# Kernel tuning notes

Hardware: AMD Instinct MI355X
Metric: run time of the kernel (lower is better)

Reference implementation:

```python
import jax, jax.numpy as jnp
import numpy as np


def setup_inputs() -> dict:
    key = jax.random.key(0)
    k = jax.random.split(key, 5)
    B, Cin, Cout, H, W = 16, 32, 32, 256, 256
    m1, m2 = 16, 16
    scale = (1.0 / (Cin * Cout)) ** 0.5  # RandomUniform limit in original
    x = jax.random.normal(k[0], (B, Cin, H, W), dtype=jnp.float32)
    ws = {
        'w1_real': jax.random.uniform(k[1], (Cin, Cout, m1, m2), jnp.float32, -scale, scale),
        'w1_imag': jax.random.uniform(k[2], (Cin, Cout, m1, m2), jnp.float32, -scale, scale),
        'w2_real': jax.random.uniform(k[3], (Cin, Cout, m1, m2), jnp.float32, -scale, scale),
        'w2_imag': jax.random.uniform(k[4], (Cin, Cout, m1, m2), jnp.float32, -scale, scale),
    }
    return {'x': x, **ws}


def reference(x, w1_real, w1_imag, w2_real, w2_imag):
    B, Cin, H, W = x.shape
    Cout, m1, m2 = w1_real.shape[1], w1_real.shape[2], w1_real.shape[3]
    Wr = W // 2 + 1
    # full rFFT2 over (H, W); x_ft: [B, Cin, H, Wr] complex64
    x_ft = jnp.fft.rfft2(x, axes=(-2, -1))
    w1 = w1_real + 1j * w1_imag  # [Cin, Cout, m1, m2]
    w2 = w2_real + 1j * w2_imag
    top = jnp.einsum('bixy,ioxy->boxy', x_ft[:, :, :m1, :m2], w1)
    bottom = jnp.einsum('bixy,ioxy->boxy', x_ft[:, :, -m1:, :m2], w2)
    out_ft = jnp.zeros((B, Cout, H, Wr), dtype=x_ft.dtype)
    out_ft = out_ft.at[:, :, :m1, :m2].set(top)
    # original pads bottom block to start at row h_ft - m1 and ADDS the two padded tensors
    out_ft = out_ft.at[:, :, H - m1:, :m2].add(bottom)
    return jnp.fft.irfft2(out_ft, s=(H, W), axes=(-2, -1))
```

## Files before the change

kernel.cpp:

```cpp
#include <hip/hip_runtime.h>
#include <math.h>


#define TWO_PI_256 0.0245436926f

typedef short short8 __attribute__((ext_vector_type(8)));
typedef float f32x4  __attribute__((ext_vector_type(4)));

__device__ __forceinline__ ushort f2bf(float v) {
    unsigned u = __float_as_uint(v);
    u += 0x7FFFu + ((u >> 16) & 1u);
    return (ushort)(u >> 16);
}
__device__ __forceinline__ float bf2f(ushort h) {
    return __uint_as_float(((unsigned)h) << 16);
}

__global__ void init_frags(ushort* __restrict__ Fr) {
    const int s = blockIdx.x;
    const int lane = threadIdx.x;
    const int q = lane >> 4, n = lane & 15;
    for (int j = 0; j < 8; ++j) {
        float v = 0.f;
        int hl;
        if (s < 32) {
            int tn = s >> 4; hl = (s >> 3) & 1; int ch = s & 7;
            int w = ch * 32 + q * 8 + j, ky = n;
            float sn, cs; __sincosf((float)((w * ky) & 255) * TWO_PI_256, &sn, &cs);
            v = tn == 0 ? cs : -sn;
        } else if (s < 160) {
            int s2 = s - 32; int mt = s2 >> 5; hl = (s2 >> 4) & 1; int ch = s2 & 15;
            int m = mt * 16 + n, k = ch * 32 + q * 8 + j;
            int kxi = m >> 1, rx = m & 1, h = k >> 1, rt = k & 1;
            int r = kxi + (kxi >= 16 ? 224 : 0);
            float sn, cs; __sincosf((float)((r * h) & 255) * TWO_PI_256, &sn, &cs);
            v = (rx == 0) ? (rt == 0 ? cs : sn) : (rt == 0 ? -sn : cs);
        } else if (s < 288) {
            int s3 = s - 160; int mtG = s3 >> 2; hl = (s3 >> 1) & 1; int ch = s3 & 1;
            int m = mtG * 16 + n, k = ch * 32 + q * 8 + j;
            int h = m >> 1, rg = m & 1, kxi = k >> 1, ry = k & 1;
            int r = kxi + (kxi >= 16 ? 224 : 0);
            float sn, cs; __sincosf((float)((r * h) & 255) * TWO_PI_256, &sn, &cs);
            v = ((rg == 0) ? (ry == 0 ? cs : -sn) : (ry == 0 ? sn : cs)) * (1.0f / 65536.0f);
        } else {
            int s4 = s - 288; int nt = s4 >> 1; hl = s4 & 1;
            int k = q * 8 + j, w = nt * 16 + n;
            int ky = k >> 1, ri = k & 1;
            float sn, cs; __sincosf((float)((w * ky) & 255) * TWO_PI_256, &sn, &cs);
            v = (ky == 0) ? (ri ? 0.f : 1.f) : (ri ? -2.f * sn : 2.f * cs);
        }
        ushort hi = f2bf(v);
        Fr[s * 512 + lane * 8 + j] = hl == 0 ? hi : f2bf(v - bf2f(hi));
    }
}

__global__ __launch_bounds__(256) void f1_gemm(const float* __restrict__ x,
                                               const ushort* __restrict__ Fr,
                                               float* __restrict__ T) {
    __shared__ ushort Ah[128 * 32], Al[128 * 32];
    const int t = threadIdx.x, blk = blockIdx.x;
    const size_t row0 = (size_t)blk * 128;
    const int bi = blk >> 1, h0 = (blk & 1) * 128;
    const int srow = t >> 3, sw4 = t & 7;
    const int lane = t & 63, wid = t >> 6, q = lane >> 4, n = lane & 15;

    f32x4 acc[2][2];
    #pragma unroll
    for (int a = 0; a < 2; ++a)
        #pragma unroll
        for (int b = 0; b < 2; ++b) acc[a][b] = (f32x4){0.f, 0.f, 0.f, 0.f};

    for (int ch = 0; ch < 8; ++ch) {
        __syncthreads();
        #pragma unroll
        for (int m = 0; m < 4; ++m) {
            const int row = srow + 32 * m;
            float4 v = *(const float4*)(x + (row0 + row) * 256 + ch * 32 + sw4 * 4);
            ushort h0_ = f2bf(v.x), h1 = f2bf(v.y), h2 = f2bf(v.z), h3 = f2bf(v.w);
            *(ushort4*)&Ah[row * 32 + sw4 * 4] = make_ushort4(h0_, h1, h2, h3);
            *(ushort4*)&Al[row * 32 + sw4 * 4] = make_ushort4(f2bf(v.x - bf2f(h0_)), f2bf(v.y - bf2f(h1)),
                                                              f2bf(v.z - bf2f(h2)), f2bf(v.w - bf2f(h3)));
        }
        __syncthreads();

        short8 bh0 = *(const short8*)&Fr[(size_t)(0  + ch) * 512 + lane * 8];
        short8 bl0 = *(const short8*)&Fr[(size_t)(8  + ch) * 512 + lane * 8];
        short8 bh1 = *(const short8*)&Fr[(size_t)(16 + ch) * 512 + lane * 8];
        short8 bl1 = *(const short8*)&Fr[(size_t)(24 + ch) * 512 + lane * 8];

        #pragma unroll
        for (int mt = 0; mt < 2; ++mt) {
            const int row = wid * 32 + mt * 16 + n;
            short8 ah = *(const short8*)&Ah[row * 32 + q * 8];
            short8 al = *(const short8*)&Al[row * 32 + q * 8];
            acc[mt][0] = __builtin_amdgcn_mfma_f32_16x16x32_bf16(al, bh0, acc[mt][0], 0, 0, 0);
            acc[mt][0] = __builtin_amdgcn_mfma_f32_16x16x32_bf16(ah, bl0, acc[mt][0], 0, 0, 0);
            acc[mt][0] = __builtin_amdgcn_mfma_f32_16x16x32_bf16(ah, bh0, acc[mt][0], 0, 0, 0);
            acc[mt][1] = __builtin_amdgcn_mfma_f32_16x16x32_bf16(al, bh1, acc[mt][1], 0, 0, 0);
            acc[mt][1] = __builtin_amdgcn_mfma_f32_16x16x32_bf16(ah, bl1, acc[mt][1], 0, 0, 0);
            acc[mt][1] = __builtin_amdgcn_mfma_f32_16x16x32_bf16(ah, bh1, acc[mt][1], 0, 0, 0);
        }
    }
    #pragma unroll
    for (int tn = 0; tn < 2; ++tn)
        #pragma unroll
        for (int mt = 0; mt < 2; ++mt)
            #pragma unroll
            for (int r = 0; r < 4; ++r) {
                int h = h0 + wid * 32 + mt * 16 + q * 4 + r;
                T[(size_t)((h * 2 + tn) * 512 + bi) * 16 + n] = acc[mt][tn][r];
            }
}

__global__ __launch_bounds__(256) void f2_gemm(const float* __restrict__ T,
                                               const ushort* __restrict__ Fr,
                                               float* __restrict__ X) {
    __shared__ ushort Bs[8 * 512];
    const int t = threadIdx.x;
    const int n0 = blockIdx.x * 64;
    const int lane = t & 63, wid = t >> 6, q = lane >> 4, nn = lane & 15;
    const int kk = t >> 3, ne = (t & 7) * 8, qk = kk >> 3, jk = kk & 7;

    f32x4 acc[4];
    #pragma unroll
    for (int m = 0; m < 4; ++m) acc[m] = (f32x4){0.f, 0.f, 0.f, 0.f};

    for (int ch = 0; ch < 16; ++ch) {
        __syncthreads();
        {
            float v[8];
            *(float4*)&v[0] = *(const float4*)&T[(size_t)(ch * 32 + kk) * 8192 + n0 + ne];
            *(float4*)&v[4] = *(const float4*)&T[(size_t)(ch * 32 + kk) * 8192 + n0 + ne + 4];
            #pragma unroll
            for (int e = 0; e < 8; ++e) {
                int nc = ne + e, nt = nc >> 4, lf = qk * 16 + (nc & 15);
                ushort hi = f2bf(v[e]);
                Bs[(nt * 2 + 0) * 512 + lf * 8 + jk] = hi;
                Bs[(nt * 2 + 1) * 512 + lf * 8 + jk] = f2bf(v[e] - bf2f(hi));
            }
        }
        __syncthreads();
        short8 bh = *(const short8*)&Bs[(wid * 2 + 0) * 512 + lane * 8];
        short8 bl = *(const short8*)&Bs[(wid * 2 + 1) * 512 + lane * 8];
        #pragma unroll
        for (int mt = 0; mt < 4; ++mt) {
            short8 ah = *(const short8*)&Fr[(size_t)(32 + mt * 32 + ch) * 512 + lane * 8];
            short8 al = *(const short8*)&Fr[(size_t)(32 + mt * 32 + 16 + ch) * 512 + lane * 8];
            acc[mt] = __builtin_amdgcn_mfma_f32_16x16x32_bf16(al, bh, acc[mt], 0, 0, 0);
            acc[mt] = __builtin_amdgcn_mfma_f32_16x16x32_bf16(ah, bl, acc[mt], 0, 0, 0);
            acc[mt] = __builtin_amdgcn_mfma_f32_16x16x32_bf16(ah, bh, acc[mt], 0, 0, 0);
        }
    }
    const int col = n0 + wid * 16 + nn;
    #pragma unroll
    for (int mt = 0; mt < 4; ++mt)
        #pragma unroll
        for (int r = 0; r < 4; ++r)
            X[(size_t)(mt * 16 + q * 4 + r) * 8192 + col] = acc[mt][r];
}

__global__ __launch_bounds__(256) void mix(const float* __restrict__ X,
                                           const float* __restrict__ w1r_, const float* __restrict__ w1i_,
                                           const float* __restrict__ w2r_, const float* __restrict__ w2i_,
                                           float* __restrict__ Y) {
    int gid = blockIdx.x * 256 + threadIdx.x;
    int ky = gid & 15, kxi = (gid >> 4) & 31, o = (gid >> 9) & 31, b = gid >> 14;
    const float* wr = (kxi < 16) ? w1r_ : w2r_;
    const float* wi = (kxi < 16) ? w1i_ : w2i_;
    int xx = kxi & 15;
    const float* Xr = X + (size_t)(kxi * 2) * 8192 + b * 512 + ky;
    const float* Xi = Xr + 8192;
    const float* wrp = wr + (size_t)(o * 16 + xx) * 16 + ky;
    const float* wip = wi + (size_t)(o * 16 + xx) * 16 + ky;
    float yr = 0.f, yi = 0.f;
    #pragma unroll 8
    for (int i = 0; i < 32; ++i) {
        float xr = Xr[i * 16], xim = Xi[i * 16];
        float wre = wrp[(size_t)i * 8192], wim = wip[(size_t)i * 8192];
        yr = fmaf(xr, wre, fmaf(-xim, wim, yr));
        yi = fmaf(xr, wim, fmaf( xim, wre, yi));
    }
    size_t yb = (size_t)(kxi * 2) * 8192 + b * 512 + o * 16 + ky;
    Y[yb] = yr;
    Y[yb + 8192] = yi;
}

__global__ __launch_bounds__(256) void i1_gemm(const float* __restrict__ Yb,
                                               const ushort* __restrict__ Fr,
                                               float* __restrict__ G) {
    __shared__ ushort Bs[8 * 512];
    const int t = threadIdx.x;
    const int Mb = blockIdx.x & 3, n0 = (blockIdx.x >> 2) * 64;
    const int lane = t & 63, wid = t >> 6, q = lane >> 4, nn = lane & 15;
    const int kk = t >> 3, ne = (t & 7) * 8, qk = kk >> 3, jk = kk & 7;

    f32x4 acc[8];
    #pragma unroll
    for (int m = 0; m < 8; ++m) acc[m] = (f32x4){0.f, 0.f, 0.f, 0.f};

    for (int ch = 0; ch < 2; ++ch) {
        __syncthreads();
        {
            float v[8];
            *(float4*)&v[0] = *(const float4*)&Yb[(size_t)(ch * 32 + kk) * 8192 + n0 + ne];
            *(float4*)&v[4] = *(const float4*)&Yb[(size_t)(ch * 32 + kk) * 8192 + n0 + ne + 4];
            #pragma unroll
            for (int e = 0; e < 8; ++e) {
                int nc = ne + e, nt = nc >> 4, lf = qk * 16 + (nc & 15);
                ushort hi = f2bf(v[e]);
                Bs[(nt * 2 + 0) * 512 + lf * 8 + jk] = hi;
                Bs[(nt * 2 + 1) * 512 + lf * 8 + jk] = f2bf(v[e] - bf2f(hi));
            }
        }
        __syncthreads();
        short8 bh = *(const short8*)&Bs[(wid * 2 + 0) * 512 + lane * 8];
        short8 bl = *(const short8*)&Bs[(wid * 2 + 1) * 512 + lane * 8];
        #pragma unroll
        for (int mt = 0; mt < 8; ++mt) {
            int mtG = Mb * 8 + mt;
            short8 ah = *(const short8*)&Fr[(size_t)(160 + mtG * 4 + ch) * 512 + lane * 8];
            short8 al = *(const short8*)&Fr[(size_t)(160 + mtG * 4 + 2 + ch) * 512 + lane * 8];
            acc[mt] = __builtin_amdgcn_mfma_f32_16x16x32_bf16(al, bh, acc[mt], 0, 0, 0);
            acc[mt] = __builtin_amdgcn_mfma_f32_16x16x32_bf16(ah, bl, acc[mt], 0, 0, 0);
            acc[mt] = __builtin_amdgcn_mfma_f32_16x16x32_bf16(ah, bh, acc[mt], 0, 0, 0);
        }
    }
    const int ncol = n0 + wid * 16 + nn;
    const int b = ncol >> 9, o = (ncol >> 4) & 31, ky = ncol & 15;
    const size_t gbase = (size_t)(b * 32 + o) * 8192 + ky * 2;
    #pragma unroll
    for (int mt = 0; mt < 8; ++mt)
        #pragma unroll
        for (int rp = 0; rp < 2; ++rp) {
            int h = (Mb * 8 + mt) * 8 + q * 2 + rp;
            *(float2*)&G[gbase + (size_t)h * 32] = make_float2(acc[mt][rp * 2], acc[mt][rp * 2 + 1]);
        }
}

__global__ __launch_bounds__(256) void i2_gemm(const float* __restrict__ G,
                                               const ushort* __restrict__ Fr,
                                               float* __restrict__ out) {
    __shared__ ushort As[8 * 512];
    const int t = threadIdx.x;
    const size_t R0 = (size_t)blockIdx.x * 64;
    const int lane = t & 63, wid = t >> 6, q = lane >> 4, nn = lane & 15;
    {
        const int row = t >> 2, qd = t & 3;
        float v[8];
        *(float4*)&v[0] = *(const float4*)&G[(R0 + row) * 32 + qd * 8];
        *(float4*)&v[4] = *(const float4*)&G[(R0 + row) * 32 + qd * 8 + 4];
        ushort hi8[8], lo8[8];
        #pragma unroll
        for (int e = 0; e < 8; ++e) {
            hi8[e] = f2bf(v[e]);
            lo8[e] = f2bf(v[e] - bf2f(hi8[e]));
        }
        const int mt = row >> 4, lf = qd * 16 + (row & 15);
        *(short8*)&As[(mt * 2 + 0) * 512 + lf * 8] = *(short8*)hi8;
        *(short8*)&As[(mt * 2 + 1) * 512 + lf * 8] = *(short8*)lo8;
    }
    __syncthreads();
    short8 ah = *(const short8*)&As[(wid * 2 + 0) * 512 + lane * 8];
    short8 al = *(const short8*)&As[(wid * 2 + 1) * 512 + lane * 8];

    f32x4 acc[16];
    #pragma unroll
    for (int m = 0; m < 16; ++m) acc[m] = (f32x4){0.f, 0.f, 0.f, 0.f};
    #pragma unroll
    for (int ntg = 0; ntg < 4; ++ntg) {
        #pragma unroll
        for (int u = 0; u < 4; ++u) {
            int nt = ntg * 4 + u;
            short8 bh = *(const short8*)&Fr[(size_t)(288 + nt * 2 + 0) * 512 + lane * 8];
            short8 bl = *(const short8*)&Fr[(size_t)(288 + nt * 2 + 1) * 512 + lane * 8];
            acc[nt] = __builtin_amdgcn_mfma_f32_16x16x32_bf16(al, bh, acc[nt], 0, 0, 0);
            acc[nt] = __builtin_amdgcn_mfma_f32_16x16x32_bf16(ah, bl, acc[nt], 0, 0, 0);
            acc[nt] = __builtin_amdgcn_mfma_f32_16x16x32_bf16(ah, bh, acc[nt], 0, 0, 0);
        }
    }
    const size_t Rrow = R0 + wid * 16 + q * 4;
    #pragma unroll
    for (int nt = 0; nt < 16; ++nt)
        #pragma unroll
        for (int r = 0; r < 4; ++r)
            out[(Rrow + r) * 256 + nt * 16 + nn] = acc[nt][r];
}

extern "C" void kernel_launch(void* const* d_in, const int* in_sizes, int n_in,
                              void* d_out, int out_size, void* d_ws, size_t ws_size,
                              hipStream_t stream) {
    const float* x   = (const float*)d_in[0];
    const float* w1r = (const float*)d_in[1];
    const float* w1i = (const float*)d_in[2];
    const float* w2r = (const float*)d_in[3];
    const float* w2i = (const float*)d_in[4];
    float* out = (float*)d_out;

    ushort* Fr = (ushort*)d_ws;
    float*  T  = (float*)((char*)d_ws + (1u << 20));
    float*  X  = T + (size_t)4194304;
    float*  Yb = X + (size_t)524288;
    float*  G  = Yb + (size_t)524288;

    init_frags<<<320,  64,  0, stream>>>(Fr);
    f1_gemm   <<<1024, 256, 0, stream>>>(x, Fr, T);
    f2_gemm   <<<128,  256, 0, stream>>>(T, Fr, X);
    mix       <<<1024, 256, 0, stream>>>(X, w1r, w1i, w2r, w2i, Yb);
    i1_gemm   <<<512,  256, 0, stream>>>(Yb, Fr, G);
    i2_gemm   <<<2048, 256, 0, stream>>>(G, Fr, out);
}
```

Baseline: 317.3 us.

## Fuse forward and inverse DFT GEMM pairs into per-image kernels via LDS

Merges the two forward DFT GEMM stages into one kernel per (batch, channel) image, and does the same for the two inverse stages. Each block now owns a whole 256x256 image with 512 threads. Intermediate spectra (T and G) stay in LDS as split bf16 hi/lo fragments instead of going through global memory, which removes the large T round trip and two launches. The cost is a bigger block with more LDS and fewer blocks (512). Half the waves sit idle in the forward second stage, and the output transform in the inverse kernel is serialized per wave.

```diff
diff --git a/kernel.cpp b/kernel.cpp
--- a/kernel.cpp
+++ b/kernel.cpp
@@ -54,28 +54,32 @@
     }
 }
 
-__global__ __launch_bounds__(256) void f1_gemm(const float* __restrict__ x,
-                                               const ushort* __restrict__ Fr,
-                                               float* __restrict__ T) {
-    __shared__ ushort Ah[128 * 32], Al[128 * 32];
-    const int t = threadIdx.x, blk = blockIdx.x;
-    const size_t row0 = (size_t)blk * 128;
-    const int bi = blk >> 1, h0 = (blk & 1) * 128;
+__global__ __launch_bounds__(512) void f12_gemm(const float* __restrict__ x,
+                                                const ushort* __restrict__ Fr,
+                                                float* __restrict__ X) {
+    __shared__ ushort LDS[16384];
+    ushort* Ah = LDS;
+    ushort* Al = LDS + 8192;
+    ushort* Ts = LDS;
+
+    const int t = threadIdx.x, bi = blockIdx.x;
+    const int lane = t & 63, w = t >> 6;
+    const int q = lane >> 4, n = lane & 15;
     const int srow = t >> 3, sw4 = t & 7;
-    const int lane = t & 63, wid = t >> 6, q = lane >> 4, n = lane & 15;
+    const float* xb = x + (size_t)bi * 65536;
 
     f32x4 acc[2][2];
     #pragma unroll
     for (int a = 0; a < 2; ++a)
         #pragma unroll
-        for (int b = 0; b < 2; ++b) acc[a][b] = (f32x4){0.f, 0.f, 0.f, 0.f};
+        for (int bb = 0; bb < 2; ++bb) acc[a][bb] = (f32x4){0.f, 0.f, 0.f, 0.f};
 
     for (int ch = 0; ch < 8; ++ch) {
         __syncthreads();
         #pragma unroll
         for (int m = 0; m < 4; ++m) {
-            const int row = srow + 32 * m;
-            float4 v = *(const float4*)(x + (row0 + row) * 256 + ch * 32 + sw4 * 4);
+            const int row = srow + 64 * m;
+            float4 v = *(const float4*)(xb + (size_t)row * 256 + ch * 32 + sw4 * 4);
             ushort h0_ = f2bf(v.x), h1 = f2bf(v.y), h2 = f2bf(v.z), h3 = f2bf(v.w);
             *(ushort4*)&Ah[row * 32 + sw4 * 4] = make_ushort4(h0_, h1, h2, h3);
             *(ushort4*)&Al[row * 32 + sw4 * 4] = make_ushort4(f2bf(v.x - bf2f(h0_)), f2bf(v.y - bf2f(h1)),
@@ -90,7 +94,7 @@
 
         #pragma unroll
         for (int mt = 0; mt < 2; ++mt) {
-            const int row = wid * 32 + mt * 16 + n;
+            const int row = w * 32 + mt * 16 + n;
             short8 ah = *(const short8*)&Ah[row * 32 + q * 8];
             short8 al = *(const short8*)&Al[row * 32 + q * 8];
             acc[mt][0] = __builtin_amdgcn_mfma_f32_16x16x32_bf16(al, bh0, acc[mt][0], 0, 0, 0);
@@ -101,62 +105,40 @@
             acc[mt][1] = __builtin_amdgcn_mfma_f32_16x16x32_bf16(ah, bh1, acc[mt][1], 0, 0, 0);
         }
     }
-    #pragma unroll
-    for (int tn = 0; tn < 2; ++tn)
-        #pragma unroll
-        for (int mt = 0; mt < 2; ++mt)
-            #pragma unroll
-            for (int r = 0; r < 4; ++r) {
-                int h = h0 + wid * 32 + mt * 16 + q * 4 + r;
-                T[(size_t)((h * 2 + tn) * 512 + bi) * 16 + n] = acc[mt][tn][r];
-            }
-}
-
-__global__ __launch_bounds__(256) void f2_gemm(const float* __restrict__ T,
-                                               const ushort* __restrict__ Fr,
-                                               float* __restrict__ X) {
-    __shared__ ushort Bs[8 * 512];
-    const int t = threadIdx.x;
-    const int n0 = blockIdx.x * 64;
-    const int lane = t & 63, wid = t >> 6, q = lane >> 4, nn = lane & 15;
-    const int kk = t >> 3, ne = (t & 7) * 8, qk = kk >> 3, jk = kk & 7;
-
-    f32x4 acc[4];
-    #pragma unroll
-    for (int m = 0; m < 4; ++m) acc[m] = (f32x4){0.f, 0.f, 0.f, 0.f};
-
-    for (int ch = 0; ch < 16; ++ch) {
-        __syncthreads();
-        {
-            float v[8];
-            *(float4*)&v[0] = *(const float4*)&T[(size_t)(ch * 32 + kk) * 8192 + n0 + ne];
-            *(float4*)&v[4] = *(const float4*)&T[(size_t)(ch * 32 + kk) * 8192 + n0 + ne + 4];
-            #pragma unroll
-            for (int e = 0; e < 8; ++e) {
-                int nc = ne + e, nt = nc >> 4, lf = qk * 16 + (nc & 15);
-                ushort hi = f2bf(v[e]);
-                Bs[(nt * 2 + 0) * 512 + lf * 8 + jk] = hi;
-                Bs[(nt * 2 + 1) * 512 + lf * 8 + jk] = f2bf(v[e] - bf2f(hi));
-            }
-        }
-        __syncthreads();
-        short8 bh = *(const short8*)&Bs[(wid * 2 + 0) * 512 + lane * 8];
-        short8 bl = *(const short8*)&Bs[(wid * 2 + 1) * 512 + lane * 8];
-        #pragma unroll
-        for (int mt = 0; mt < 4; ++mt) {
-            short8 ah = *(const short8*)&Fr[(size_t)(32 + mt * 32 + ch) * 512 + lane * 8];
-            short8 al = *(const short8*)&Fr[(size_t)(32 + mt * 32 + 16 + ch) * 512 + lane * 8];
-            acc[mt] = __builtin_amdgcn_mfma_f32_16x16x32_bf16(al, bh, acc[mt], 0, 0, 0);
-            acc[mt] = __builtin_amdgcn_mfma_f32_16x16x32_bf16(ah, bl, acc[mt], 0, 0, 0);
-            acc[mt] = __builtin_amdgcn_mfma_f32_16x16x32_bf16(ah, bh, acc[mt], 0, 0, 0);
-        }
-    }
-    const int col = n0 + wid * 16 + nn;
-    #pragma unroll
-    for (int mt = 0; mt < 4; ++mt)
+
+    __syncthreads();
+    #pragma unroll
+    for (int mt = 0; mt < 2; ++mt) {
+        ushort h8[8], l8[8];
+        #pragma unroll
+        for (int j = 0; j < 8; ++j) {
+            float v = acc[mt][j & 1][j >> 1];
+            h8[j] = f2bf(v);
+            l8[j] = f2bf(v - bf2f(h8[j]));
+        }
+        const int c = w * 2 + mt;
+        *(short8*)&Ts[c * 1024 + lane * 8]       = *(short8*)h8;
+        *(short8*)&Ts[c * 1024 + 512 + lane * 8] = *(short8*)l8;
+    }
+    __syncthreads();
+
+    if (w < 4) {
+        const int mt2 = w;
+        f32x4 a2 = (f32x4){0.f, 0.f, 0.f, 0.f};
+        #pragma unroll
+        for (int c2 = 0; c2 < 16; ++c2) {
+            short8 bh = *(const short8*)&Ts[c2 * 1024 + lane * 8];
+            short8 bl = *(const short8*)&Ts[c2 * 1024 + 512 + lane * 8];
+            short8 ah = *(const short8*)&Fr[(size_t)(32 + mt2 * 32 + c2) * 512 + lane * 8];
+            short8 al = *(const short8*)&Fr[(size_t)(32 + mt2 * 32 + 16 + c2) * 512 + lane * 8];
+            a2 = __builtin_amdgcn_mfma_f32_16x16x32_bf16(al, bh, a2, 0, 0, 0);
+            a2 = __builtin_amdgcn_mfma_f32_16x16x32_bf16(ah, bl, a2, 0, 0, 0);
+            a2 = __builtin_amdgcn_mfma_f32_16x16x32_bf16(ah, bh, a2, 0, 0, 0);
+        }
         #pragma unroll
         for (int r = 0; r < 4; ++r)
-            X[(size_t)(mt * 16 + q * 4 + r) * 8192 + col] = acc[mt][r];
+            X[(size_t)(mt2 * 16 + q * 4 + r) * 8192 + bi * 16 + n] = a2[r];
+    }
 }
 
 __global__ __launch_bounds__(256) void mix(const float* __restrict__ X,
@@ -185,105 +167,88 @@
     Y[yb + 8192] = yi;
 }
 
-__global__ __launch_bounds__(256) void i1_gemm(const float* __restrict__ Yb,
-                                               const ushort* __restrict__ Fr,
-                                               float* __restrict__ G) {
-    __shared__ ushort Bs[8 * 512];
-    const int t = threadIdx.x;
-    const int Mb = blockIdx.x & 3, n0 = (blockIdx.x >> 2) * 64;
-    const int lane = t & 63, wid = t >> 6, q = lane >> 4, nn = lane & 15;
-    const int kk = t >> 3, ne = (t & 7) * 8, qk = kk >> 3, jk = kk & 7;
-
-    f32x4 acc[8];
-    #pragma unroll
-    for (int m = 0; m < 8; ++m) acc[m] = (f32x4){0.f, 0.f, 0.f, 0.f};
-
+__global__ __launch_bounds__(512) void i12_gemm(const float* __restrict__ Yb,
+                                                const ushort* __restrict__ Fr,
+                                                float* __restrict__ out) {
+    __shared__ ushort Bs[2048];
+    __shared__ ushort As[16384];
+    const int t = threadIdx.x, bo = blockIdx.x;
+    const int lane = t & 63, w = t >> 6;
+    const int q = lane >> 4, n = lane & 15;
+    const int b = bo >> 5, o = bo & 31;
+
+    if (t < 256) {
+        const int k = t >> 2, e4 = t & 3;
+        float4 v = *(const float4*)&Yb[(size_t)k * 8192 + b * 512 + o * 16 + e4 * 4];
+        const int c = k >> 5, q2 = (k >> 3) & 3, j2 = k & 7;
+        float vv[4] = {v.x, v.y, v.z, v.w};
+        #pragma unroll
+        for (int ee = 0; ee < 4; ++ee) {
+            const int ky = e4 * 4 + ee;
+            ushort hi = f2bf(vv[ee]);
+            Bs[c * 1024 + (q2 * 16 + ky) * 8 + j2]       = hi;
+            Bs[c * 1024 + 512 + (q2 * 16 + ky) * 8 + j2] = f2bf(vv[ee] - bf2f(hi));
+        }
+    }
+    __syncthreads();
+
+    f32x4 g[4];
+    #pragma unroll
+    for (int mi = 0; mi < 4; ++mi) g[mi] = (f32x4){0.f, 0.f, 0.f, 0.f};
+    #pragma unroll
     for (int ch = 0; ch < 2; ++ch) {
-        __syncthreads();
-        {
-            float v[8];
-            *(float4*)&v[0] = *(const float4*)&Yb[(size_t)(ch * 32 + kk) * 8192 + n0 + ne];
-            *(float4*)&v[4] = *(const float4*)&Yb[(size_t)(ch * 32 + kk) * 8192 + n0 + ne + 4];
-            #pragma unroll
-            for (int e = 0; e < 8; ++e) {
-                int nc = ne + e, nt = nc >> 4, lf = qk * 16 + (nc & 15);
-                ushort hi = f2bf(v[e]);
-                Bs[(nt * 2 + 0) * 512 + lf * 8 + jk] = hi;
-                Bs[(nt * 2 + 1) * 512 + lf * 8 + jk] = f2bf(v[e] - bf2f(hi));
-            }
-        }
-        __syncthreads();
-        short8 bh = *(const short8*)&Bs[(wid * 2 + 0) * 512 + lane * 8];
-        short8 bl = *(const short8*)&Bs[(wid * 2 + 1) * 512 + lane * 8];
-        #pragma unroll
-        for (int mt = 0; mt < 8; ++mt) {
-            int mtG = Mb * 8 + mt;
+        short8 bh = *(const short8*)&Bs[ch * 1024 + lane * 8];
+        short8 bl = *(const short8*)&Bs[ch * 1024 + 512 + lane * 8];
+        #pragma unroll
+        for (int mi = 0; mi < 4; ++mi) {
+            const int mtG = w * 4 + mi;
             short8 ah = *(const short8*)&Fr[(size_t)(160 + mtG * 4 + ch) * 512 + lane * 8];
             short8 al = *(const short8*)&Fr[(size_t)(160 + mtG * 4 + 2 + ch) * 512 + lane * 8];
-            acc[mt] = __builtin_amdgcn_mfma_f32_16x16x32_bf16(al, bh, acc[mt], 0, 0, 0);
-            acc[mt] = __builtin_amdgcn_mfma_f32_16x16x32_bf16(ah, bl, acc[mt], 0, 0, 0);
-            acc[mt] = __builtin_amdgcn_mfma_f32_16x16x32_bf16(ah, bh, acc[mt], 0, 0, 0);
-        }
-    }
-    const int ncol = n0 + wid * 16 + nn;
-    const int b = ncol >> 9, o = (ncol >> 4) & 31, ky = ncol & 15;
-    const size_t gbase = (size_t)(b * 32 + o) * 8192 + ky * 2;
-    #pragma unroll
-    for (int mt = 0; mt < 8; ++mt)
-        #pragma unroll
-        for (int rp = 0; rp < 2; ++rp) {
-            int h = (Mb * 8 + mt) * 8 + q * 2 + rp;
-            *(float2*)&G[gbase + (size_t)h * 32] = make_float2(acc[mt][rp * 2], acc[mt][rp * 2 + 1]);
-        }
-}
-
-__global__ __launch_bounds__(256) void i2_gemm(const float* __restrict__ G,
-                                               const ushort* __restrict__ Fr,
-                                               float* __restrict__ out) {
-    __shared__ ushort As[8 * 512];
-    const int t = threadIdx.x;
-    const size_t R0 = (size_t)blockIdx.x * 64;
-    const int lane = t & 63, wid = t >> 6, q = lane >> 4, nn = lane & 15;
-    {
-        const int row = t >> 2, qd = t & 3;
-        float v[8];
-        *(float4*)&v[0] = *(const float4*)&G[(R0 + row) * 32 + qd * 8];
-        *(float4*)&v[4] = *(const float4*)&G[(R0 + row) * 32 + qd * 8 + 4];
-        ushort hi8[8], lo8[8];
-        #pragma unroll
-        for (int e = 0; e < 8; ++e) {
-            hi8[e] = f2bf(v[e]);
-            lo8[e] = f2bf(v[e] - bf2f(hi8[e]));
-        }
-        const int mt = row >> 4, lf = qd * 16 + (row & 15);
-        *(short8*)&As[(mt * 2 + 0) * 512 + lf * 8] = *(short8*)hi8;
-        *(short8*)&As[(mt * 2 + 1) * 512 + lf * 8] = *(short8*)lo8;
-    }
-    __syncthreads();
-    short8 ah = *(const short8*)&As[(wid * 2 + 0) * 512 + lane * 8];
-    short8 al = *(const short8*)&As[(wid * 2 + 1) * 512 + lane * 8];
-
-    f32x4 acc[16];
-    #pragma unroll
-    for (int m = 0; m < 16; ++m) acc[m] = (f32x4){0.f, 0.f, 0.f, 0.f};
-    #pragma unroll
-    for (int ntg = 0; ntg < 4; ++ntg) {
-        #pragma unroll
-        for (int u = 0; u < 4; ++u) {
-            int nt = ntg * 4 + u;
-            short8 bh = *(const short8*)&Fr[(size_t)(288 + nt * 2 + 0) * 512 + lane * 8];
+            g[mi] = __builtin_amdgcn_mfma_f32_16x16x32_bf16(al, bh, g[mi], 0, 0, 0);
+            g[mi] = __builtin_amdgcn_mfma_f32_16x16x32_bf16(ah, bl, g[mi], 0, 0, 0);
+            g[mi] = __builtin_amdgcn_mfma_f32_16x16x32_bf16(ah, bh, g[mi], 0, 0, 0);
+        }
+    }
+
+    #pragma unroll
+    for (int mi = 0; mi < 4; ++mi)
+        #pragma unroll
+        for (int r = 0; r < 4; ++r) {
+            const int m1 = (w * 4 + mi) * 16 + q * 4 + r;
+            const int h = m1 >> 1, ri = m1 & 1;
+            const int k2 = 2 * n + ri;
+            const int ht = h >> 4, hr = h & 15;
+            const int ad = ((k2 >> 3) * 16 + hr) * 8 + (k2 & 7);
+            const float v = g[mi][r];
+            const ushort hi = f2bf(v);
+            As[ht * 1024 + ad]       = hi;
+            As[ht * 1024 + 512 + ad] = f2bf(v - bf2f(hi));
+        }
+    __syncthreads();
+
+    #pragma unroll
+    for (int mi2 = 0; mi2 < 2; ++mi2) {
+        const int ht2 = w * 2 + mi2;
+        short8 ah = *(const short8*)&As[ht2 * 1024 + lane * 8];
+        short8 al = *(const short8*)&As[ht2 * 1024 + 512 + lane * 8];
+        f32x4 a3[16];
+        #pragma unroll
+        for (int nt = 0; nt < 16; ++nt) a3[nt] = (f32x4){0.f, 0.f, 0.f, 0.f};
+        #pragma unroll
+        for (int nt = 0; nt < 16; ++nt) {
+            short8 bh = *(const short8*)&Fr[(size_t)(288 + nt * 2) * 512 + lane * 8];
             short8 bl = *(const short8*)&Fr[(size_t)(288 + nt * 2 + 1) * 512 + lane * 8];
-            acc[nt] = __builtin_amdgcn_mfma_f32_16x16x32_bf16(al, bh, acc[nt], 0, 0, 0);
-            acc[nt] = __builtin_amdgcn_mfma_f32_16x16x32_bf16(ah, bl, acc[nt], 0, 0, 0);
-            acc[nt] = __builtin_amdgcn_mfma_f32_16x16x32_bf16(ah, bh, acc[nt], 0, 0, 0);
-        }
-    }
-    const size_t Rrow = R0 + wid * 16 + q * 4;
-    #pragma unroll
-    for (int nt = 0; nt < 16; ++nt)
-        #pragma unroll
-        for (int r = 0; r < 4; ++r)
-            out[(Rrow + r) * 256 + nt * 16 + nn] = acc[nt][r];
+            a3[nt] = __builtin_amdgcn_mfma_f32_16x16x32_bf16(al, bh, a3[nt], 0, 0, 0);
+            a3[nt] = __builtin_amdgcn_mfma_f32_16x16x32_bf16(ah, bl, a3[nt], 0, 0, 0);
+            a3[nt] = __builtin_amdgcn_mfma_f32_16x16x32_bf16(ah, bh, a3[nt], 0, 0, 0);
+        }
+        const size_t Rrow = (size_t)bo * 256 + ht2 * 16 + q * 4;
+        #pragma unroll
+        for (int nt = 0; nt < 16; ++nt)
+            #pragma unroll
+            for (int r = 0; r < 4; ++r)
+                out[(Rrow + r) * 256 + nt * 16 + n] = a3[nt][r];
+    }
 }
 
 extern "C" void kernel_launch(void* const* d_in, const int* in_sizes, int n_in,
@@ -297,15 +262,11 @@
     float* out = (float*)d_out;
 
     ushort* Fr = (ushort*)d_ws;
-    float*  T  = (float*)((char*)d_ws + (1u << 20));
-    float*  X  = T + (size_t)4194304;
+    float*  X  = (float*)((char*)d_ws + (1u << 20));
     float*  Yb = X + (size_t)524288;
-    float*  G  = Yb + (size_t)524288;
 
     init_frags<<<320,  64,  0, stream>>>(Fr);
-    f1_gemm   <<<1024, 256, 0, stream>>>(x, Fr, T);
-    f2_gemm   <<<128,  256, 0, stream>>>(T, Fr, X);
+    f12_gemm  <<<512,  512, 0, stream>>>(x, Fr, X);
     mix       <<<1024, 256, 0, stream>>>(X, w1r, w1i, w2r, w2i, Yb);
-    i1_gemm   <<<512,  256, 0, stream>>>(Yb, Fr, G);
-    i2_gemm   <<<2048, 256, 0, stream>>>(G, Fr, out);
-}
+    i12_gemm  <<<512,  512, 0, stream>>>(Yb, Fr, out);
+}
```

New measurement: 273.9 us. -13.7%, faster.
